# Performance work log

Hardware: AMD Instinct MI355X
Metric: run time of the kernel (lower is better)

## Reference

```python
import jax, jax.numpy as jnp
import numpy as np

N_OSC = 60
B = 65536
DT = 0.1
STEPS = 10
PHI_INV = 2.0 / (1.0 + np.sqrt(5.0))


def setup_inputs() -> dict:
    key = jax.random.key(0)
    k1, k2, k3 = jax.random.split(key, 3)
    theta = jax.random.uniform(k1, (B, N_OSC), dtype=jnp.float32) * (2.0 * np.pi) - np.pi
    K = jax.random.normal(k2, (N_OSC, N_OSC), dtype=jnp.float32) * 0.1
    omega = jax.random.normal(k3, (N_OSC,), dtype=jnp.float32) * 0.1
    return {
        'theta': theta,
        'K': K,
        'omega': omega,
        'K_global': jnp.float32(PHI_INV),
        'coupling_mod': jnp.float32(0.6),        # phase_coupling['quasi_crystal']
        'neg_entropy_gate': jnp.float32(0.5),
        'critical_slow_factor': jnp.float32(0.1),
        'delta_s_neg': jnp.float32(0.8),          # NegativeEntropyState constant
        'relaxation_time': jnp.float32(5.0),      # NegativeEntropyState constant
    }


def reference(theta, K, omega, K_global, coupling_mod, neg_entropy_gate,
              critical_slow_factor, delta_s_neg, relaxation_time):
    n = theta.shape[-1]
    K_eff = K * coupling_mod                               # [n, n]
    critical_factor = 1.0 / (1.0 + critical_slow_factor * relaxation_time)
    eff_dt = DT * critical_factor
    boost = 1.0 + neg_entropy_gate * delta_s_neg
    scale = K_global * boost / n

    def step(th, _):
        # theta_diff[b, i, j] = th[b, j] - th[b, i]
        diff = th[..., None, :] - th[..., :, None]          # [B, n, n]
        coupling_sum = jnp.sum(K_eff * jnp.sin(diff), axis=-1)  # [B, n]
        th = th + eff_dt * (omega + scale * coupling_sum)
        th = jnp.arctan2(jnp.sin(th), jnp.cos(th))          # wrap to (-pi, pi]
        return th, None

    theta, _ = jax.lax.scan(step, theta, None, length=STEPS)
    cos_m = jnp.cos(theta).mean(axis=-1)
    sin_m = jnp.sin(theta).mean(axis=-1)
    coherence = jnp.sqrt(cos_m ** 2 + sin_m ** 2)           # [B]
    return theta, coherence
```

## Files before the change

kernel.cpp:

```cpp
#include <hip/hip_runtime.h>
#include <stdint.h>
#include <math.h>


#define B_TOTAL 65536
#define NOSC 60
#define STEPS 10

using short4v = __attribute__((ext_vector_type(4))) short;
using floatx4 = __attribute__((ext_vector_type(4))) float;

#if __has_builtin(__builtin_amdgcn_perm)
__device__ __forceinline__ unsigned int perm_b32(unsigned int s0, unsigned int s1, unsigned int sel) {
    return __builtin_amdgcn_perm(s0, s1, sel);
}
#else
__device__ __forceinline__ unsigned int perm_b32(unsigned int s0, unsigned int s1, unsigned int sel) {
    unsigned long long pool = ((unsigned long long)s0 << 32) | s1;
    unsigned int r = 0;
#pragma unroll
    for (int b = 0; b < 4; ++b) {
        unsigned int s = (sel >> (8 * b)) & 0xff;
        r |= ((unsigned int)((pool >> (8 * s)) & 0xff)) << (8 * b);
    }
    return r;
}
#endif

__device__ __forceinline__ unsigned int fbits(float x)        { return __builtin_bit_cast(unsigned int, x); }
__device__ __forceinline__ float        bitsf(unsigned int u) { return __builtin_bit_cast(float, u); }

#if __has_builtin(__builtin_amdgcn_mfma_f32_16x16x16bf16_1k)
__device__ __forceinline__ floatx4 mfma16(short4v a, short4v b, floatx4 c) {
    return __builtin_amdgcn_mfma_f32_16x16x16bf16_1k(a, b, c, 0, 0, 0);
}
#else
__device__ __forceinline__ floatx4 mfma16(short4v a, short4v b, floatx4 c) {
    asm("v_mfma_f32_16x16x16_bf16 %0, %1, %2, %0" : "+v"(c) : "v"(a), "v"(b));
    return c;
}
#endif

__device__ __forceinline__ unsigned int pack_hi_pair(float a, float b) {
    return perm_b32(fbits(b), fbits(a), 0x07060302u);
}

__global__ __launch_bounds__(256)
void kuramoto_kernel(const float* __restrict__ theta_in,
                     const float* __restrict__ Kmat,
                     const float* __restrict__ omega,
                     const float* __restrict__ p_kglobal,
                     const float* __restrict__ p_cmod,
                     const float* __restrict__ p_gate,
                     const float* __restrict__ p_slow,
                     const float* __restrict__ p_dsneg,
                     const float* __restrict__ p_relax,
                     float* __restrict__ theta_out,
                     float* __restrict__ coh_out)
{
    const int lane = threadIdx.x & 63;
    const int wid  = threadIdx.x >> 6;
    const int lidx = lane & 15;
    const int quad = lane >> 4;

    const float kglobal = p_kglobal[0];
    const float cmod    = p_cmod[0];
    const float gate    = p_gate[0];
    const float slow    = p_slow[0];
    const float dsneg   = p_dsneg[0];
    const float relax   = p_relax[0];

    float eff_dt, scale;
    {
#pragma clang fp contract(off)
        const float a     = slow * relax;
        const float b     = 1.0f + a;
        const float crit  = 1.0f / b;
        eff_dt            = 0.1f * crit;
        const float boost = 1.0f + gate * dsneg;
        scale             = (kglobal * boost) / 60.0f;
    }

    const int batch0 = (blockIdx.x * 4 + wid) * 16;
    const int brow   = (batch0 + lidx) * NOSC;

    short4v AH[4][4], AL[4][4];
#pragma unroll
    for (int nt = 0; nt < 4; ++nt) {
        const int i = nt * 16 + lidx;
        const bool okn = (i < NOSC);
#pragma unroll
        for (int kt = 0; kt < 4; ++kt) {
            const int k0 = kt * 16 + quad * 4;
            float kv[4];
            if (okn && (k0 + 3) < NOSC) {
                const float4 a = *(const float4*)(Kmat + i * NOSC + k0);
                kv[0] = a.x; kv[1] = a.y; kv[2] = a.z; kv[3] = a.w;
            } else {
#pragma unroll
                for (int j = 0; j < 4; ++j)
                    kv[j] = (okn && (k0 + j) < NOSC) ? Kmat[i * NOSC + k0 + j] : 0.0f;
            }
            short4v h, l;
#pragma unroll
            for (int j = 0; j < 4; ++j) {
                const float v = kv[j] * cmod;
                const unsigned int hb = fbits(v) & 0xffff0000u;
                const float rlo = v - bitsf(hb);
                h[j] = (short)(hb >> 16);
                l[j] = (short)(fbits(rlo) >> 16);
            }
            AH[nt][kt] = h;
            AL[nt][kt] = l;
        }
    }

    float th[4][4], sn[4][4], cn[4][4], omg[4][4];
#pragma unroll
    for (int nt = 0; nt < 4; ++nt) {
        const int o0 = nt * 16 + quad * 4;
        if (o0 + 3 < NOSC) {
            const float4 tv = *(const float4*)(theta_in + brow + o0);
            const float4 ov = *(const float4*)(omega + o0);
            th[nt][0] = tv.x; th[nt][1] = tv.y; th[nt][2] = tv.z; th[nt][3] = tv.w;
            omg[nt][0] = ov.x; omg[nt][1] = ov.y; omg[nt][2] = ov.z; omg[nt][3] = ov.w;
        } else {
#pragma unroll
            for (int r = 0; r < 4; ++r) { th[nt][r] = 0.0f; omg[nt][r] = 0.0f; }
        }
#pragma unroll
        for (int r = 0; r < 4; ++r)
            __sincosf(th[nt][r], &sn[nt][r], &cn[nt][r]);
    }

    const float PI_F = 3.14159274101257324f;
    const float C_HI = 6.28318548202514648f;
    const float C_LO = -1.7484556e-7f;

    for (int t = 0; t < STEPS; ++t) {
        floatx4 accS[4], accC[4];
#pragma unroll
        for (int nt = 0; nt < 4; ++nt) { accS[nt] = (floatx4)0.0f; accC[nt] = (floatx4)0.0f; }

#pragma unroll
        for (int kt = 0; kt < 4; ++kt) {
            union PU { unsigned int u[2]; short4v v; };
            PU bsh, bsl, bch, bcl;
            float slo[4], clo[4];
#pragma unroll
            for (int r = 0; r < 4; ++r) {
                const unsigned int us = fbits(sn[kt][r]);
                slo[r] = sn[kt][r] - bitsf(us & 0xffff0000u);
                const unsigned int uc = fbits(cn[kt][r]);
                clo[r] = cn[kt][r] - bitsf(uc & 0xffff0000u);
            }
            bsh.u[0] = pack_hi_pair(sn[kt][0], sn[kt][1]);
            bsh.u[1] = pack_hi_pair(sn[kt][2], sn[kt][3]);
            bsl.u[0] = pack_hi_pair(slo[0], slo[1]);
            bsl.u[1] = pack_hi_pair(slo[2], slo[3]);
            bch.u[0] = pack_hi_pair(cn[kt][0], cn[kt][1]);
            bch.u[1] = pack_hi_pair(cn[kt][2], cn[kt][3]);
            bcl.u[0] = pack_hi_pair(clo[0], clo[1]);
            bcl.u[1] = pack_hi_pair(clo[2], clo[3]);

#pragma unroll
            for (int nt = 0; nt < 4; ++nt) accS[nt] = mfma16(AH[nt][kt], bsh.v, accS[nt]);
#pragma unroll
            for (int nt = 0; nt < 4; ++nt) accC[nt] = mfma16(AH[nt][kt], bch.v, accC[nt]);
#pragma unroll
            for (int nt = 0; nt < 4; ++nt) accS[nt] = mfma16(AL[nt][kt], bsh.v, accS[nt]);
#pragma unroll
            for (int nt = 0; nt < 4; ++nt) accC[nt] = mfma16(AL[nt][kt], bch.v, accC[nt]);
#pragma unroll
            for (int nt = 0; nt < 4; ++nt) accS[nt] = mfma16(AH[nt][kt], bsl.v, accS[nt]);
#pragma unroll
            for (int nt = 0; nt < 4; ++nt) accC[nt] = mfma16(AH[nt][kt], bcl.v, accC[nt]);
        }

#pragma unroll
        for (int nt = 0; nt < 4; ++nt) {
#pragma unroll
            for (int r = 0; r < 4; ++r) {
                const float S = accS[nt][r];
                const float C = accC[nt][r];
                const float coup = cn[nt][r] * S - sn[nt][r] * C;
                float nth;
                {
#pragma clang fp contract(off)
                    const float t1 = scale * coup;
                    const float t2 = omg[nt][r] + t1;
                    const float t3 = eff_dt * t2;
                    nth = th[nt][r] + t3;
                }
                float n = 0.0f;
                n = (nth >=  PI_F) ?  1.0f : n;
                n = (nth <= -PI_F) ? -1.0f : n;
                float y = fmaf(n, -C_HI, nth);
                y = fmaf(n, -C_LO, y);
                th[nt][r] = y;
                __sincosf(y, &sn[nt][r], &cn[nt][r]);
            }
        }
    }

#pragma unroll
    for (int nt = 0; nt < 4; ++nt) {
        const int o0 = nt * 16 + quad * 4;
        if (o0 + 3 < NOSC) {
            float4 tv;
            tv.x = th[nt][0]; tv.y = th[nt][1]; tv.z = th[nt][2]; tv.w = th[nt][3];
            *(float4*)(theta_out + brow + o0) = tv;
        }
    }

    float pc = 0.0f, ps = 0.0f;
#pragma unroll
    for (int nt = 0; nt < 4; ++nt) {
        if (nt * 16 + quad * 4 < NOSC) {
#pragma unroll
            for (int r = 0; r < 4; ++r) { pc += cn[nt][r]; ps += sn[nt][r]; }
        }
    }
    pc += __shfl_xor(pc, 16);
    ps += __shfl_xor(ps, 16);
    pc += __shfl_xor(pc, 32);
    ps += __shfl_xor(ps, 32);
    if (quad == 0) {
        const float cm = pc / 60.0f;
        const float sm = ps / 60.0f;
        coh_out[batch0 + lidx] = sqrtf(cm * cm + sm * sm);
    }
}

extern "C" void kernel_launch(void* const* d_in, const int* in_sizes, int n_in,
                              void* d_out, int out_size, void* d_ws, size_t ws_size,
                              hipStream_t stream) {
    const float* theta = (const float*)d_in[0];
    const float* Kmat  = (const float*)d_in[1];
    const float* omg   = (const float*)d_in[2];
    const float* kg    = (const float*)d_in[3];
    const float* cmod  = (const float*)d_in[4];
    const float* gate  = (const float*)d_in[5];
    const float* slow  = (const float*)d_in[6];
    const float* dsn   = (const float*)d_in[7];
    const float* relax = (const float*)d_in[8];
    float* out = (float*)d_out;

    kuramoto_kernel<<<dim3(B_TOTAL / 64), dim3(256), 0, stream>>>(
        theta, Kmat, omg, kg, cmod, gate, slow, dsn, relax,
        out, out + (size_t)B_TOTAL * NOSC);
}
```

Baseline: 128.0 us.

## Ping-pong two batch tiles per wave to overlap MFMA with sincos updates

```diff
diff --git a/kernel.cpp b/kernel.cpp
--- a/kernel.cpp
+++ b/kernel.cpp
@@ -45,7 +45,82 @@
     return perm_b32(fbits(b), fbits(a), 0x07060302u);
 }
 
-__global__ __launch_bounds__(256)
+__device__ __forceinline__ void mfma_tile(const short4v (&AH)[4][4], const short4v (&AL)[4][4],
+                                          const float (&sn)[4][4], const float (&cn)[4][4],
+                                          floatx4 (&accS)[4], floatx4 (&accC)[4])
+{
+    const floatx4 Z = (floatx4)0.0f;
+#pragma unroll
+    for (int kt = 0; kt < 4; ++kt) {
+        union PU { unsigned int u[2]; short4v v; };
+        PU bsh, bsl, bch, bcl;
+        float slo[4], clo[4];
+#pragma unroll
+        for (int r = 0; r < 4; ++r) {
+            const unsigned int us = fbits(sn[kt][r]);
+            slo[r] = sn[kt][r] - bitsf(us & 0xffff0000u);
+            const unsigned int uc = fbits(cn[kt][r]);
+            clo[r] = cn[kt][r] - bitsf(uc & 0xffff0000u);
+        }
+        bsh.u[0] = pack_hi_pair(sn[kt][0], sn[kt][1]);
+        bsh.u[1] = pack_hi_pair(sn[kt][2], sn[kt][3]);
+        bsl.u[0] = pack_hi_pair(slo[0], slo[1]);
+        bsl.u[1] = pack_hi_pair(slo[2], slo[3]);
+        bch.u[0] = pack_hi_pair(cn[kt][0], cn[kt][1]);
+        bch.u[1] = pack_hi_pair(cn[kt][2], cn[kt][3]);
+        bcl.u[0] = pack_hi_pair(clo[0], clo[1]);
+        bcl.u[1] = pack_hi_pair(clo[2], clo[3]);
+
+#pragma unroll
+        for (int nt = 0; nt < 4; ++nt) accS[nt] = mfma16(AH[nt][kt], bsh.v, (kt == 0) ? Z : accS[nt]);
+#pragma unroll
+        for (int nt = 0; nt < 4; ++nt) accC[nt] = mfma16(AH[nt][kt], bch.v, (kt == 0) ? Z : accC[nt]);
+#pragma unroll
+        for (int nt = 0; nt < 4; ++nt) accS[nt] = mfma16(AL[nt][kt], bsh.v, accS[nt]);
+#pragma unroll
+        for (int nt = 0; nt < 4; ++nt) accC[nt] = mfma16(AL[nt][kt], bch.v, accC[nt]);
+#pragma unroll
+        for (int nt = 0; nt < 4; ++nt) accS[nt] = mfma16(AH[nt][kt], bsl.v, accS[nt]);
+#pragma unroll
+        for (int nt = 0; nt < 4; ++nt) accC[nt] = mfma16(AH[nt][kt], bcl.v, accC[nt]);
+    }
+}
+
+__device__ __forceinline__ void update_tile(float (&th)[4][4], float (&sn)[4][4], float (&cn)[4][4],
+                                            const float (&omg)[4][4],
+                                            const floatx4 (&accS)[4], const floatx4 (&accC)[4],
+                                            float scale, float eff_dt)
+{
+    const float PI_F = 3.14159274101257324f;
+    const float C_HI = 6.28318548202514648f;
+    const float C_LO = -1.7484556e-7f;
+#pragma unroll
+    for (int nt = 0; nt < 4; ++nt) {
+#pragma unroll
+        for (int r = 0; r < 4; ++r) {
+            const float S = accS[nt][r];
+            const float C = accC[nt][r];
+            const float coup = cn[nt][r] * S - sn[nt][r] * C;
+            float nth;
+            {
+#pragma clang fp contract(off)
+                const float t1 = scale * coup;
+                const float t2 = omg[nt][r] + t1;
+                const float t3 = eff_dt * t2;
+                nth = th[nt][r] + t3;
+            }
+            float n = 0.0f;
+            n = (nth >=  PI_F) ?  1.0f : n;
+            n = (nth <= -PI_F) ? -1.0f : n;
+            float y = fmaf(n, -C_HI, nth);
+            y = fmaf(n, -C_LO, y);
+            th[nt][r] = y;
+            __sincosf(y, &sn[nt][r], &cn[nt][r]);
+        }
+    }
+}
+
+__global__ __launch_bounds__(64)
 void kuramoto_kernel(const float* __restrict__ theta_in,
                      const float* __restrict__ Kmat,
                      const float* __restrict__ omega,
@@ -59,7 +134,6 @@
                      float* __restrict__ coh_out)
 {
     const int lane = threadIdx.x & 63;
-    const int wid  = threadIdx.x >> 6;
     const int lidx = lane & 15;
     const int quad = lane >> 4;
 
@@ -81,8 +155,10 @@
         scale             = (kglobal * boost) / 60.0f;
     }
 
-    const int batch0 = (blockIdx.x * 4 + wid) * 16;
-    const int brow   = (batch0 + lidx) * NOSC;
+    const int batch0A = blockIdx.x * 32;
+    const int batch0B = batch0A + 16;
+    const int browA   = (batch0A + lidx) * NOSC;
+    const int browB   = (batch0B + lidx) * NOSC;
 
     short4v AH[4][4], AL[4][4];
 #pragma unroll
@@ -115,120 +191,78 @@
         }
     }
 
-    float th[4][4], sn[4][4], cn[4][4], omg[4][4];
+    float thA[4][4], snA[4][4], cnA[4][4];
+    float thB[4][4], snB[4][4], cnB[4][4];
+    float omg[4][4];
 #pragma unroll
     for (int nt = 0; nt < 4; ++nt) {
         const int o0 = nt * 16 + quad * 4;
         if (o0 + 3 < NOSC) {
-            const float4 tv = *(const float4*)(theta_in + brow + o0);
             const float4 ov = *(const float4*)(omega + o0);
-            th[nt][0] = tv.x; th[nt][1] = tv.y; th[nt][2] = tv.z; th[nt][3] = tv.w;
             omg[nt][0] = ov.x; omg[nt][1] = ov.y; omg[nt][2] = ov.z; omg[nt][3] = ov.w;
+            const float4 ta = *(const float4*)(theta_in + browA + o0);
+            thA[nt][0] = ta.x; thA[nt][1] = ta.y; thA[nt][2] = ta.z; thA[nt][3] = ta.w;
+            const float4 tb = *(const float4*)(theta_in + browB + o0);
+            thB[nt][0] = tb.x; thB[nt][1] = tb.y; thB[nt][2] = tb.z; thB[nt][3] = tb.w;
         } else {
 #pragma unroll
-            for (int r = 0; r < 4; ++r) { th[nt][r] = 0.0f; omg[nt][r] = 0.0f; }
-        }
-#pragma unroll
-        for (int r = 0; r < 4; ++r)
-            __sincosf(th[nt][r], &sn[nt][r], &cn[nt][r]);
-    }
-
-    const float PI_F = 3.14159274101257324f;
-    const float C_HI = 6.28318548202514648f;
-    const float C_LO = -1.7484556e-7f;
-
-    for (int t = 0; t < STEPS; ++t) {
-        floatx4 accS[4], accC[4];
-#pragma unroll
-        for (int nt = 0; nt < 4; ++nt) { accS[nt] = (floatx4)0.0f; accC[nt] = (floatx4)0.0f; }
-
-#pragma unroll
-        for (int kt = 0; kt < 4; ++kt) {
-            union PU { unsigned int u[2]; short4v v; };
-            PU bsh, bsl, bch, bcl;
-            float slo[4], clo[4];
-#pragma unroll
             for (int r = 0; r < 4; ++r) {
-                const unsigned int us = fbits(sn[kt][r]);
-                slo[r] = sn[kt][r] - bitsf(us & 0xffff0000u);
-                const unsigned int uc = fbits(cn[kt][r]);
-                clo[r] = cn[kt][r] - bitsf(uc & 0xffff0000u);
-            }
-            bsh.u[0] = pack_hi_pair(sn[kt][0], sn[kt][1]);
-            bsh.u[1] = pack_hi_pair(sn[kt][2], sn[kt][3]);
-            bsl.u[0] = pack_hi_pair(slo[0], slo[1]);
-            bsl.u[1] = pack_hi_pair(slo[2], slo[3]);
-            bch.u[0] = pack_hi_pair(cn[kt][0], cn[kt][1]);
-            bch.u[1] = pack_hi_pair(cn[kt][2], cn[kt][3]);
-            bcl.u[0] = pack_hi_pair(clo[0], clo[1]);
-            bcl.u[1] = pack_hi_pair(clo[2], clo[3]);
-
-#pragma unroll
-            for (int nt = 0; nt < 4; ++nt) accS[nt] = mfma16(AH[nt][kt], bsh.v, accS[nt]);
-#pragma unroll
-            for (int nt = 0; nt < 4; ++nt) accC[nt] = mfma16(AH[nt][kt], bch.v, accC[nt]);
-#pragma unroll
-            for (int nt = 0; nt < 4; ++nt) accS[nt] = mfma16(AL[nt][kt], bsh.v, accS[nt]);
-#pragma unroll
-            for (int nt = 0; nt < 4; ++nt) accC[nt] = mfma16(AL[nt][kt], bch.v, accC[nt]);
-#pragma unroll
-            for (int nt = 0; nt < 4; ++nt) accS[nt] = mfma16(AH[nt][kt], bsl.v, accS[nt]);
-#pragma unroll
-            for (int nt = 0; nt < 4; ++nt) accC[nt] = mfma16(AH[nt][kt], bcl.v, accC[nt]);
-        }
-
-#pragma unroll
-        for (int nt = 0; nt < 4; ++nt) {
-#pragma unroll
-            for (int r = 0; r < 4; ++r) {
-                const float S = accS[nt][r];
-                const float C = accC[nt][r];
-                const float coup = cn[nt][r] * S - sn[nt][r] * C;
-                float nth;
-                {
-#pragma clang fp contract(off)
-                    const float t1 = scale * coup;
-                    const float t2 = omg[nt][r] + t1;
-                    const float t3 = eff_dt * t2;
-                    nth = th[nt][r] + t3;
-                }
-                float n = 0.0f;
-                n = (nth >=  PI_F) ?  1.0f : n;
-                n = (nth <= -PI_F) ? -1.0f : n;
-                float y = fmaf(n, -C_HI, nth);
-                y = fmaf(n, -C_LO, y);
-                th[nt][r] = y;
-                __sincosf(y, &sn[nt][r], &cn[nt][r]);
-            }
-        }
-    }
+                omg[nt][r] = 0.0f; thA[nt][r] = 0.0f; thB[nt][r] = 0.0f;
+            }
+        }
+#pragma unroll
+        for (int r = 0; r < 4; ++r) {
+            __sincosf(thA[nt][r], &snA[nt][r], &cnA[nt][r]);
+            __sincosf(thB[nt][r], &snB[nt][r], &cnB[nt][r]);
+        }
+    }
+
+    floatx4 accSA[4], accCA[4], accSB[4], accCB[4];
+
+    mfma_tile(AH, AL, snA, cnA, accSA, accCA);
+#pragma unroll 1
+    for (int t = 0; t < STEPS - 1; ++t) {
+        mfma_tile(AH, AL, snB, cnB, accSB, accCB);
+        update_tile(thA, snA, cnA, omg, accSA, accCA, scale, eff_dt);
+        mfma_tile(AH, AL, snA, cnA, accSA, accCA);
+        update_tile(thB, snB, cnB, omg, accSB, accCB, scale, eff_dt);
+    }
+    mfma_tile(AH, AL, snB, cnB, accSB, accCB);
+    update_tile(thA, snA, cnA, omg, accSA, accCA, scale, eff_dt);
+    update_tile(thB, snB, cnB, omg, accSB, accCB, scale, eff_dt);
 
 #pragma unroll
     for (int nt = 0; nt < 4; ++nt) {
         const int o0 = nt * 16 + quad * 4;
         if (o0 + 3 < NOSC) {
-            float4 tv;
-            tv.x = th[nt][0]; tv.y = th[nt][1]; tv.z = th[nt][2]; tv.w = th[nt][3];
-            *(float4*)(theta_out + brow + o0) = tv;
-        }
-    }
-
-    float pc = 0.0f, ps = 0.0f;
+            float4 ta, tb;
+            ta.x = thA[nt][0]; ta.y = thA[nt][1]; ta.z = thA[nt][2]; ta.w = thA[nt][3];
+            *(float4*)(theta_out + browA + o0) = ta;
+            tb.x = thB[nt][0]; tb.y = thB[nt][1]; tb.z = thB[nt][2]; tb.w = thB[nt][3];
+            *(float4*)(theta_out + browB + o0) = tb;
+        }
+    }
+
+    float pcA = 0.0f, psA = 0.0f, pcB = 0.0f, psB = 0.0f;
 #pragma unroll
     for (int nt = 0; nt < 4; ++nt) {
         if (nt * 16 + quad * 4 < NOSC) {
 #pragma unroll
-            for (int r = 0; r < 4; ++r) { pc += cn[nt][r]; ps += sn[nt][r]; }
-        }
-    }
-    pc += __shfl_xor(pc, 16);
-    ps += __shfl_xor(ps, 16);
-    pc += __shfl_xor(pc, 32);
-    ps += __shfl_xor(ps, 32);
+            for (int r = 0; r < 4; ++r) {
+                pcA += cnA[nt][r]; psA += snA[nt][r];
+                pcB += cnB[nt][r]; psB += snB[nt][r];
+            }
+        }
+    }
+    pcA += __shfl_xor(pcA, 16); psA += __shfl_xor(psA, 16);
+    pcA += __shfl_xor(pcA, 32); psA += __shfl_xor(psA, 32);
+    pcB += __shfl_xor(pcB, 16); psB += __shfl_xor(psB, 16);
+    pcB += __shfl_xor(pcB, 32); psB += __shfl_xor(psB, 32);
     if (quad == 0) {
-        const float cm = pc / 60.0f;
-        const float sm = ps / 60.0f;
-        coh_out[batch0 + lidx] = sqrtf(cm * cm + sm * sm);
+        const float cmA = pcA / 60.0f, smA = psA / 60.0f;
+        coh_out[batch0A + lidx] = sqrtf(cmA * cmA + smA * smA);
+        const float cmB = pcB / 60.0f, smB = psB / 60.0f;
+        coh_out[batch0B + lidx] = sqrtf(cmB * cmB + smB * smB);
     }
 }
 
@@ -246,7 +280,7 @@
     const float* relax = (const float*)d_in[8];
     float* out = (float*)d_out;
 
-    kuramoto_kernel<<<dim3(B_TOTAL / 64), dim3(256), 0, stream>>>(
+    kuramoto_kernel<<<dim3(B_TOTAL / 32), dim3(64), 0, stream>>>(
         theta, Kmat, omg, kg, cmod, gate, slow, dsn, relax,
         out, out + (size_t)B_TOTAL * NOSC);
 }
```

Result: no change. 126.1 us (-1.5%).
